# Optimization experiments

Hardware: AMD Instinct MI355X
Metric: run time of the kernel (lower is better)

Reference implementation:

```python
import jax, jax.numpy as jnp
import numpy as np

N_IN, M_MID = 512, 256
B, H, W = 16, 64, 64

def setup_inputs() -> dict:
    key = jax.random.key(0)
    ks = jax.random.split(key, 7)
    s = 0.05
    return {
        "x": jax.random.normal(ks[0], (B, N_IN, H, W), dtype=jnp.float32),
        "W_state": jax.random.normal(ks[1], (M_MID, N_IN), dtype=jnp.float32) * s,
        "b_state": jax.random.normal(ks[2], (M_MID,), dtype=jnp.float32) * s,
        "W_proj": jax.random.normal(ks[3], (M_MID, N_IN), dtype=jnp.float32) * s,
        "b_proj": jax.random.normal(ks[4], (M_MID,), dtype=jnp.float32) * s,
        "W_extend": jax.random.normal(ks[5], (N_IN, M_MID), dtype=jnp.float32) * s,
        "b_extend": jax.random.normal(ks[6], (N_IN,), dtype=jnp.float32) * s,
    }

def reference(x, W_state, b_state, W_proj, b_proj, W_extend, b_extend):
    n, c, h, w = x.shape
    hw = h * w
    xf = x.reshape(n, c, hw)                                   # [n, C, HW]
    # 1x1 convs are channel GEMMs over flattened spatial dim
    x_state = jnp.einsum('mc,nch->nmh', W_state, xf) + b_state[None, :, None]   # [n, M, HW]
    x_proj = jnp.einsum('mc,nch->nmh', W_proj, xf) + b_proj[None, :, None]      # [n, M, HW]
    # bmm -> scale -> softmax -> bmm (graph reasoning over M x M)
    scores = jnp.einsum('nmh,nkh->nmk', x_state, x_proj) / jnp.sqrt(jnp.float32(hw))
    attn = jax.nn.softmax(scores, axis=2)                      # [n, M, M]
    x_rstate = jnp.einsum('nmk,nkh->nmh', attn, x_proj)        # [n, M, HW]
    # extend back to C channels + residual
    ext = jnp.einsum('cm,nmh->nch', W_extend, x_rstate) + b_extend[None, :, None]
    return x + ext.reshape(n, c, h, w)
```

## Files before the change

kernel.cpp:

```cpp
#include <hip/hip_runtime.h>
#include <hip/hip_bf16.h>
#include <stdint.h>

typedef __bf16 bf16x8_t __attribute__((ext_vector_type(8)));
typedef float  f32x4_t  __attribute__((ext_vector_type(4)));
typedef short  short8_t __attribute__((ext_vector_type(8)));

__device__ __forceinline__ unsigned short f2b(float f) {
    union { float f; unsigned u; } v; v.f = f;
    unsigned u = v.u;
    return (unsigned short)((u + 0x7FFFu + ((u >> 16) & 1u)) >> 16);
}
__device__ __forceinline__ float b2f(unsigned short b) {
    union { unsigned u; float f; } v; v.u = ((unsigned)b) << 16; return v.f;
}

#define AS3(p) ((__attribute__((address_space(3))) void*)(p))
#define AS1(p) ((const __attribute__((address_space(1))) void*)(p))
#define FENCE() asm volatile("" ::: "memory")

#define NB   16
#define CIN  512
#define MMID 256
#define HW   4096
#define KSPLIT 4
#define ASZ  (128 * 64)
#define ASZA3 (256 * 64)
#define ASZB3 (64 * 64)

__device__ __forceinline__ void swz3(int gx, int gy, int& bx, int& by, int& bz) {
    const int nwg = gridDim.x, ord = blockIdx.x, q = nwg >> 3;
    const int s = (ord & 7) * q + (ord >> 3);
    by = s % gy;
    const int rem = s / gy;
    bx = rem % gx;
    bz = rem / gx;
}

__global__ __launch_bounds__(256) void prep_weights(
    const float* __restrict__ Ws, const float* __restrict__ Wp,
    const float* __restrict__ Wef, const float* __restrict__ bs,
    const float* __restrict__ bp,
    unsigned short* __restrict__ Wsp, unsigned short* __restrict__ Wex,
    unsigned short* __restrict__ WpT, float* __restrict__ bsp)
{
    int i = blockIdx.x * 256 + threadIdx.x;
    if (i < MMID * CIN) {
        Wsp[i]              = f2b(Ws[i]);
        Wsp[MMID * CIN + i] = f2b(Wp[i]);
        Wex[i]              = f2b(Wef[i]);
        const int c = i >> 8, k = i & (MMID - 1);
        WpT[i] = f2b(Wp[(size_t)k * CIN + c]);
    }
    if (i < MMID) { bsp[i] = bs[i]; bsp[MMID + i] = bp[i]; }
}

__global__ __launch_bounds__(256) void transpose_convert_x(
    const float* __restrict__ x, unsigned short* __restrict__ xT)
{
    __shared__ unsigned short tile[64][66];
    const int n = blockIdx.z, c0 = blockIdx.y * 64, h0 = blockIdx.x * 64;
    const float* s = x + ((size_t)n * CIN + c0) * HW + h0;
    unsigned short* d = xT + ((size_t)n * HW + h0) * CIN + c0;
    const int t = threadIdx.x;
    {
        const int rr = t >> 4, cc = (t & 15) * 4;
        #pragma unroll
        for (int p = 0; p < 4; ++p) {
            int r = p * 16 + rr;
            float4 v = *(const float4*)(s + (size_t)r * HW + cc);
            tile[r][cc + 0] = f2b(v.x); tile[r][cc + 1] = f2b(v.y);
            tile[r][cc + 2] = f2b(v.z); tile[r][cc + 3] = f2b(v.w);
        }
    }
    __syncthreads();
    {
        const int wr = t >> 3, wc = (t & 7) * 8;
        #pragma unroll
        for (int p = 0; p < 2; ++p) {
            int h = p * 32 + wr;
            unsigned short tmp[8];
            #pragma unroll
            for (int j = 0; j < 8; ++j) tmp[j] = tile[wc + j][h];
            *(short8_t*)(d + (size_t)h * CIN + wc) = *(const short8_t*)tmp;
        }
    }
}

__global__ __launch_bounds__(256) void transpose_bf16_64(
    const unsigned short* __restrict__ src, unsigned short* __restrict__ dst,
    int srs, int drs, long long sbs, long long dbs)
{
    __shared__ unsigned short tile[64][66];
    const int n = blockIdx.z, r0 = blockIdx.y * 64, c0 = blockIdx.x * 64;
    const unsigned short* s = src + (size_t)n * sbs + (size_t)r0 * srs + c0;
    unsigned short* d = dst + (size_t)n * dbs + (size_t)c0 * drs + r0;
    const int t = threadIdx.x;
    const int rr = t >> 3, cc = (t & 7) * 8;
    #pragma unroll
    for (int p = 0; p < 2; ++p) {
        int r = p * 32 + rr;
        short8_t v = *(const short8_t*)(s + (size_t)r * srs + cc);
        #pragma unroll
        for (int j = 0; j < 8; ++j) tile[r][cc + j] = ((const unsigned short*)&v)[j];
    }
    __syncthreads();
    #pragma unroll
    for (int p = 0; p < 2; ++p) {
        int c = p * 32 + rr;
        unsigned short tmp[8];
        #pragma unroll
        for (int j = 0; j < 8; ++j) tmp[j] = tile[cc + j][c];
        *(short8_t*)(d + (size_t)c * drs + cc) = *(const short8_t*)tmp;
    }
}

template <int EPI>
__device__ __forceinline__ void epilogue_repack(
    f32x4_t (&acc)[4][4], unsigned short* smem,
    int m0, int n0, int wave, int lane,
    void* __restrict__ Cout, int ldc, size_t cbase)
{
    float* fbuf = (float*)smem;
    const int t   = wave * 64 + lane;
    const int l15 = lane & 15, l16 = lane >> 4;
    const int wr2 = wave >> 1;
    const int wc  = (wave & 1) * 64;

    #pragma unroll
    for (int p = 0; p < 4; ++p) {
        __syncthreads();
        if (wr2 == (p >> 1)) {
            const int ihalf = p & 1;
            #pragma unroll
            for (int i2 = 0; i2 < 2; ++i2) {
                const int i = ihalf * 2 + i2;
                #pragma unroll
                for (int r = 0; r < 4; ++r) {
                    const int lrow = i2 * 16 + l16 * 4 + r;
                    #pragma unroll
                    for (int j = 0; j < 4; ++j)
                        fbuf[lrow * 132 + wc + j * 16 + l15] = acc[i][j][r];
                }
            }
        }
        __syncthreads();
        #pragma unroll
        for (int it = 0; it < 2; ++it) {
            const int lrow = it * 16 + (t >> 4);
            const int col  = (t & 15) * 8;
            const int row  = m0 + p * 32 + lrow;
            float v[8];
            *(float4*)&v[0] = *(const float4*)&fbuf[lrow * 132 + col];
            *(float4*)&v[4] = *(const float4*)&fbuf[lrow * 132 + col + 4];
            const size_t idx = cbase + (size_t)row * ldc + n0 + col;
            if constexpr (EPI == 1) {
                float* op = (float*)Cout + idx;
                *(float4*)op = *(const float4*)&v[0];
                *(float4*)(op + 4) = *(const float4*)&v[4];
            } else if constexpr (EPI == 4) {
                unsigned short o[8];
                #pragma unroll
                for (int k = 0; k < 8; ++k)
                    o[k] = f2b(v[k] + ((row == n0 + col + k) ? 1.0f : 0.0f));
                *(short8_t*)((unsigned short*)Cout + idx) = *(const short8_t*)o;
            } else {
                unsigned short o[8];
                #pragma unroll
                for (int k = 0; k < 8; ++k) o[k] = f2b(v[k]);
                *(short8_t*)((unsigned short*)Cout + idx) = *(const short8_t*)o;
            }
        }
    }
}

#define GEMM_KLOOP(Ab, Bb, lda, ldb, KBEG, NT)                                          \
    auto stage = [&](int k0, int b) {                                                   \
        unsigned short* Asb = smem + b * 2 * ASZ;                                       \
        unsigned short* Bsb = Asb + ASZ;                                                \
        _Pragma("unroll")                                                               \
        for (int c = 0; c < 4; ++c) {                                                   \
            const int o   = (c * 256 + t) * 16;                                         \
            const int row = o >> 7;                                                     \
            const int ce  = ((o & 127) ^ ((row & 7) << 4)) >> 1;                        \
            __builtin_amdgcn_global_load_lds(                                           \
                AS1(Ab + (size_t)row * lda + k0 + ce), AS3((char*)Asb + o), 16, 0, 0);  \
            __builtin_amdgcn_global_load_lds(                                           \
                AS1(Bb + (size_t)row * ldb + k0 + ce), AS3((char*)Bsb + o), 16, 0, 0);  \
        }                                                                               \
    };                                                                                  \
    stage(KBEG, 0);                                                                     \
    for (int itk = 0; itk < (NT); ++itk) {                                              \
        const int cur = itk & 1;                                                        \
        if (itk + 1 < (NT)) {                                                           \
            stage(KBEG + (itk + 1) * 64, cur ^ 1);                                      \
            asm volatile("s_waitcnt vmcnt(8)" ::: "memory");                            \
        } else {                                                                        \
            asm volatile("s_waitcnt vmcnt(0)" ::: "memory");                            \
        }                                                                               \
        __builtin_amdgcn_s_barrier();                                                   \
        FENCE();                                                                        \
        const char* Asb = (const char*)(smem + cur * 2 * ASZ);                          \
        const char* Bsb = Asb + 2 * ASZ;                                                \
        const int swz = (l15 & 7) << 4;                                                 \
        _Pragma("unroll")                                                               \
        for (int ks = 0; ks < 2; ++ks) {                                                \
            bf16x8_t af[4], bfr[4];                                                     \
            const int cb = (ks * 64 + l16 * 16) ^ swz;                                  \
            _Pragma("unroll")                                                           \
            for (int i = 0; i < 4; ++i) {                                               \
                af[i]  = *(const bf16x8_t*)(Asb + (wr + i * 16 + l15) * 128 + cb);      \
                bfr[i] = *(const bf16x8_t*)(Bsb + (wc + i * 16 + l15) * 128 + cb);      \
            }                                                                           \
            _Pragma("unroll")                                                           \
            for (int i = 0; i < 4; ++i)                                                 \
                _Pragma("unroll")                                                       \
                for (int j = 0; j < 4; ++j)                                             \
                    acc[i][j] = __builtin_amdgcn_mfma_f32_16x16x32_bf16(                \
                        af[i], bfr[j], acc[i][j], 0, 0, 0);                             \
        }                                                                               \
        FENCE();                                                                        \
        __builtin_amdgcn_s_barrier();                                                   \
        FENCE();                                                                        \
    }

template <int EPI>
__global__ __launch_bounds__(256, 2) void gemm_occ2(
    const unsigned short* __restrict__ A, const unsigned short* __restrict__ B,
    long long strideA, long long strideB,
    const float* __restrict__ bias, int bias_bstride,
    void* __restrict__ Cout, int ldc, long long strideC,
    int gx, int gy)
{
    __shared__ unsigned short smem[2 * (ASZA3 + ASZB3)];

    int bx, by, n;  swz3(gx, gy, bx, by, n);
    const int m0 = by * 256;
    const int n0 = bx * 64;

    const unsigned short* Ab = A + (size_t)n * strideA + (size_t)m0 * CIN;
    const unsigned short* Bb = B + (size_t)n * strideB + (size_t)n0 * CIN;

    const int t    = threadIdx.x;
    const int lane = t & 63;
    const int wave = t >> 6;
    const int wr   = wave * 64;
    const int l15  = lane & 15;
    const int l16  = lane >> 4;

    f32x4_t acc[4][4] = {};

    auto stage = [&](int k0, int b) {
        unsigned short* Asb = smem + b * (ASZA3 + ASZB3);
        unsigned short* Bsb = Asb + ASZA3;
        #pragma unroll
        for (int c = 0; c < 8; ++c) {
            const int o   = (c * 256 + t) * 16;
            const int row = o >> 7;
            const int ce  = ((o & 127) ^ ((row & 7) << 4)) >> 1;
            __builtin_amdgcn_global_load_lds(
                AS1(Ab + (size_t)row * CIN + k0 + ce), AS3((char*)Asb + o), 16, 0, 0);
        }
        #pragma unroll
        for (int c = 0; c < 2; ++c) {
            const int o   = (c * 256 + t) * 16;
            const int row = o >> 7;
            const int ce  = ((o & 127) ^ ((row & 7) << 4)) >> 1;
            __builtin_amdgcn_global_load_lds(
                AS1(Bb + (size_t)row * CIN + k0 + ce), AS3((char*)Bsb + o), 16, 0, 0);
        }
    };

    const int NT = CIN / 64;
    stage(0, 0);
    for (int itk = 0; itk < NT; ++itk) {
        const int cur = itk & 1;
        if (itk + 1 < NT) {
            stage((itk + 1) * 64, cur ^ 1);
            asm volatile("s_waitcnt vmcnt(10)" ::: "memory");
        } else {
            asm volatile("s_waitcnt vmcnt(0)" ::: "memory");
        }
        __builtin_amdgcn_s_barrier();
        FENCE();
        const char* Asb = (const char*)(smem + cur * (ASZA3 + ASZB3));
        const char* Bsb = Asb + 2 * ASZA3;
        const int swz = (l15 & 7) << 4;
        #pragma unroll
        for (int ks = 0; ks < 2; ++ks) {
            const int cb = (ks * 64 + l16 * 16) ^ swz;
            bf16x8_t af[4], bfr[4];
            #pragma unroll
            for (int i = 0; i < 4; ++i)
                af[i] = *(const bf16x8_t*)(Asb + (wr + i * 16 + l15) * 128 + cb);
            #pragma unroll
            for (int j = 0; j < 4; ++j)
                bfr[j] = *(const bf16x8_t*)(Bsb + (j * 16 + l15) * 128 + cb);
            #pragma unroll
            for (int i = 0; i < 4; ++i)
                #pragma unroll
                for (int j = 0; j < 4; ++j)
                    acc[i][j] = __builtin_amdgcn_mfma_f32_16x16x32_bf16(
                        af[i], bfr[j], acc[i][j], 0, 0, 0);
        }
        FENCE();
        __builtin_amdgcn_s_barrier();
        FENCE();
    }

    float* fbuf = (float*)smem;
    const size_t cbase = (size_t)n * strideC;
    const float* beff = bias + (size_t)n * bias_bstride;
    #pragma unroll
    for (int p = 0; p < 8; ++p) {
        __syncthreads();
        if (wave == (p >> 1)) {
            #pragma unroll
            for (int i2 = 0; i2 < 2; ++i2) {
                const int i = (p & 1) * 2 + i2;
                #pragma unroll
                for (int r = 0; r < 4; ++r) {
                    const int lrow = i2 * 16 + l16 * 4 + r;
                    #pragma unroll
                    for (int j = 0; j < 4; ++j)
                        fbuf[lrow * 68 + j * 16 + l15] = acc[i][j][r];
                }
            }
        }
        __syncthreads();
        const int lrow = t >> 3;
        const int col  = (t & 7) * 8;
        const int row  = m0 + p * 32 + lrow;
        float v[8];
        *(float4*)&v[0] = *(const float4*)&fbuf[lrow * 68 + col];
        *(float4*)&v[4] = *(const float4*)&fbuf[lrow * 68 + col + 4];
        const float badd = beff[row];
        const size_t idx = cbase + (size_t)row * ldc + n0 + col;
        if constexpr (EPI == 1) {
            float o[8];
            #pragma unroll
            for (int k = 0; k < 8; ++k) o[k] = v[k] + badd;
            float* op = (float*)Cout + idx;
            *(float4*)op = *(const float4*)&o[0];
            *(float4*)(op + 4) = *(const float4*)&o[4];
        } else {
            unsigned short o[8];
            #pragma unroll
            for (int k = 0; k < 8; ++k) o[k] = f2b(v[k] + badd);
            *(short8_t*)((unsigned short*)Cout + idx) = *(const short8_t*)o;
        }
    }
}

__global__ __launch_bounds__(256) void gemm_scores(
    const unsigned short* __restrict__ Ysp, float* __restrict__ scoresP)
{
    __shared__ unsigned short smem[4 * ASZ];

    int bx, by, z;  swz3(MMID / 128, MMID / 128, bx, by, z);
    const int n  = z >> 2;
    const int kc = z & 3;
    const int m0 = by * 128;
    const int n0 = bx * 128;

    const unsigned short* Ab = Ysp + (size_t)n * CIN * HW + (size_t)m0 * HW;
    const unsigned short* Bb = Ysp + (size_t)n * CIN * HW + (size_t)(MMID + n0) * HW;

    const int t    = threadIdx.x;
    const int lane = t & 63;
    const int wave = t >> 6;
    const int wr   = (wave >> 1) * 64;
    const int wc   = (wave & 1) * 64;
    const int l15  = lane & 15;
    const int l16  = lane >> 4;

    f32x4_t acc[4][4] = {};
    const int kbeg = kc * (HW / KSPLIT);
    GEMM_KLOOP(Ab, Bb, HW, HW, kbeg, (HW / KSPLIT) / 64)

    float* outp = scoresP + (size_t)(kc * NB + n) * MMID * MMID;
    epilogue_repack<1>(acc, smem, m0, n0, wave, lane, outp, MMID, 0);
}

__global__ __launch_bounds__(256) void softmax_rows(
    const float* __restrict__ scoresP, unsigned short* __restrict__ attn)
{
    const int wave = threadIdx.x >> 6;
    const int l    = threadIdx.x & 63;
    const size_t row = (size_t)blockIdx.x * 4 + wave;
    const size_t pstride = (size_t)NB * MMID * MMID;
    float4 v = {0.f, 0.f, 0.f, 0.f};
    #pragma unroll
    for (int p = 0; p < KSPLIT; ++p) {
        float4 u = *(const float4*)(scoresP + p * pstride + row * MMID + l * 4);
        v.x += u.x; v.y += u.y; v.z += u.z; v.w += u.w;
    }
    float mx = fmaxf(fmaxf(v.x, v.y), fmaxf(v.z, v.w));
    #pragma unroll
    for (int off = 32; off; off >>= 1) mx = fmaxf(mx, __shfl_xor(mx, off));
    const float sc = 0.015625f;
    float e0 = __expf((v.x - mx) * sc), e1 = __expf((v.y - mx) * sc);
    float e2 = __expf((v.z - mx) * sc), e3 = __expf((v.w - mx) * sc);
    float sum = e0 + e1 + e2 + e3;
    #pragma unroll
    for (int off = 32; off; off >>= 1) sum += __shfl_xor(sum, off);
    const float inv = 1.0f / sum;
    unsigned short o[4] = { f2b(e0 * inv), f2b(e1 * inv), f2b(e2 * inv), f2b(e3 * inv) };
    *(uint64_t*)(attn + row * MMID + l * 4) = *(const uint64_t*)o;
}

__global__ __launch_bounds__(256) void compute_vec(
    const unsigned short* __restrict__ G, const float* __restrict__ bsp,
    const float* __restrict__ be, float* __restrict__ vec)
{
    const int n = blockIdx.x >> 1;
    const int c = ((blockIdx.x & 1) << 8) + threadIdx.x;
    const unsigned short* g = G + ((size_t)n * CIN + c) * MMID;
    float s = 0.f;
    for (int k = 0; k < MMID; k += 8) {
        short8_t v = *(const short8_t*)(g + k);
        #pragma unroll
        for (int j = 0; j < 8; ++j)
            s += b2f((unsigned short)v[j]) * bsp[MMID + k + j];
    }
    vec[n * CIN + c] = be[c] + s;
}

template <int EPI>
__global__ __launch_bounds__(256) void gemm_nt(
    const unsigned short* __restrict__ A, const unsigned short* __restrict__ B,
    int lda, int ldb, int K,
    long long strideA, long long strideB,
    void* __restrict__ Cout, int ldc, long long strideC,
    int gx, int gy)
{
    __shared__ unsigned short smem[4 * ASZ];

    int bx, by, n;  swz3(gx, gy, bx, by, n);
    const int m0 = by * 128;
    const int n0 = bx * 128;

    const unsigned short* Ab = A + (size_t)n * strideA + (size_t)m0 * lda;
    const unsigned short* Bb = B + (size_t)n * strideB + (size_t)n0 * ldb;

    const int t    = threadIdx.x;
    const int lane = t & 63;
    const int wave = t >> 6;
    const int wr   = (wave >> 1) * 64;
    const int wc   = (wave & 1) * 64;
    const int l15  = lane & 15;
    const int l16  = lane >> 4;

    f32x4_t acc[4][4] = {};
    GEMM_KLOOP(Ab, Bb, lda, ldb, 0, K / 64)

    epilogue_repack<EPI>(acc, smem, m0, n0, wave, lane,
                         Cout, ldc, (size_t)n * strideC);
}

extern "C" void kernel_launch(void* const* d_in, const int* in_sizes, int n_in,
                              void* d_out, int out_size, void* d_ws, size_t ws_size,
                              hipStream_t stream)
{
    const float* x   = (const float*)d_in[0];
    const float* Ws  = (const float*)d_in[1];
    const float* bs  = (const float*)d_in[2];
    const float* Wp  = (const float*)d_in[3];
    const float* bp  = (const float*)d_in[4];
    const float* Wef = (const float*)d_in[5];
    const float* be  = (const float*)d_in[6];
    float* out = (float*)d_out;

    unsigned short* xT   = (unsigned short*)d_ws;
    unsigned short* Ysp  = xT   + (size_t)NB * HW * CIN;
    unsigned short* Wsp  = Ysp  + (size_t)NB * CIN * HW;
    unsigned short* Wex  = Wsp  + (size_t)CIN * CIN;
    unsigned short* WpT  = Wex  + (size_t)CIN * MMID;
    unsigned short* attn = WpT  + (size_t)CIN * MMID;
    unsigned short* attnT= attn + (size_t)NB * MMID * MMID;
    unsigned short* G    = attnT+ (size_t)NB * MMID * MMID;
    unsigned short* Meff = G    + (size_t)NB * CIN * MMID;
    float* scoresP = (float*)(Meff + (size_t)NB * CIN * CIN);
    float* bsp = scoresP + (size_t)KSPLIT * NB * MMID * MMID;
    float* vec = bsp + CIN;

    prep_weights<<<512, 256, 0, stream>>>(Ws, Wp, Wef, bs, bp, Wsp, Wex, WpT, bsp);

    transpose_convert_x<<<dim3(HW / 64, CIN / 64, NB), 256, 0, stream>>>(x, xT);

    gemm_occ2<0><<<(CIN / 256) * (HW / 64) * NB, 256, 0, stream>>>(
        Wsp, xT, 0LL, (long long)HW * CIN,
        bsp, 0, Ysp, HW, (long long)CIN * HW,
        HW / 64, CIN / 256);

    gemm_scores<<<(MMID / 128) * (MMID / 128) * NB * KSPLIT, 256, 0, stream>>>(
        Ysp, scoresP);

    softmax_rows<<<NB * MMID / 4, 256, 0, stream>>>(scoresP, attn);

    transpose_bf16_64<<<dim3(MMID / 64, MMID / 64, NB), 256, 0, stream>>>(
        attn, attnT, MMID, MMID, (long long)MMID * MMID, (long long)MMID * MMID);

    gemm_nt<2><<<(MMID / 128) * (CIN / 128) * NB, 256, 0, stream>>>(
        Wex, attnT, MMID, MMID, MMID,
        0LL, (long long)MMID * MMID,
        G, MMID, (long long)CIN * MMID,
        MMID / 128, CIN / 128);

    compute_vec<<<NB * 2, 256, 0, stream>>>(G, bsp, be, vec);

    gemm_nt<4><<<(CIN / 128) * (CIN / 128) * NB, 256, 0, stream>>>(
        G, WpT, MMID, MMID, MMID,
        (long long)CIN * MMID, 0LL,
        Meff, CIN, (long long)CIN * CIN,
        CIN / 128, CIN / 128);

    gemm_occ2<1><<<(CIN / 256) * (HW / 64) * NB, 256, 0, stream>>>(
        Meff, xT, (long long)CIN * CIN, (long long)HW * CIN,
        vec, CIN, out, HW, (long long)CIN * HW,
        HW / 64, CIN / 256);
}
```

Measured before the change: 197.4 us.

## Keep B tile stationary in LDS and stream A from global per wave

The two big channel GEMMs are replaced by a kernel that loads the whole 64-column x 512-K slice of B into LDS once and covers all 512 output rows per block with 8 waves. Each wave streams its A fragments directly from global memory (L2-resident weights) instead of staging them through double-buffered LDS. This removes the per-k-step barriers and redundant B reloads across row tiles and halves the grid. The cost is 64KB of LDS per block and uncoalesced direct global A loads with no prefetching, and __launch_bounds__(512,4) may put pressure on registers.

Result: slower. 260.7 us (+32.1%).

```diff
diff --git a/kernel.cpp b/kernel.cpp
--- a/kernel.cpp
+++ b/kernel.cpp
@@ -25,8 +25,6 @@
 #define HW   4096
 #define KSPLIT 4
 #define ASZ  (128 * 64)
-#define ASZA3 (256 * 64)
-#define ASZB3 (64 * 64)
 
 __device__ __forceinline__ void swz3(int gx, int gy, int& bx, int& by, int& bz) {
     const int nwg = gridDim.x, ord = blockIdx.x, q = nwg >> 3;
@@ -225,129 +223,97 @@
     }
 
 template <int EPI>
-__global__ __launch_bounds__(256, 2) void gemm_occ2(
+__global__ __launch_bounds__(512, 4) void gemm_bstat(
     const unsigned short* __restrict__ A, const unsigned short* __restrict__ B,
     long long strideA, long long strideB,
     const float* __restrict__ bias, int bias_bstride,
-    void* __restrict__ Cout, int ldc, long long strideC,
-    int gx, int gy)
-{
-    __shared__ unsigned short smem[2 * (ASZA3 + ASZB3)];
-
-    int bx, by, n;  swz3(gx, gy, bx, by, n);
-    const int m0 = by * 256;
+    void* __restrict__ Cout, int ldc, long long strideC, int gx)
+{
+    __shared__ unsigned short smem[64 * 512];
+
+    int bx, by, n;  swz3(gx, 1, bx, by, n);
     const int n0 = bx * 64;
 
-    const unsigned short* Ab = A + (size_t)n * strideA + (size_t)m0 * CIN;
     const unsigned short* Bb = B + (size_t)n * strideB + (size_t)n0 * CIN;
 
     const int t    = threadIdx.x;
     const int lane = t & 63;
     const int wave = t >> 6;
-    const int wr   = wave * 64;
     const int l15  = lane & 15;
     const int l16  = lane >> 4;
 
+    #pragma unroll
+    for (int c = 0; c < 8; ++c) {
+        const int o   = (c * 512 + t) * 16;
+        const int row = o >> 10;
+        const int ce  = ((o & 1023) ^ ((row & 7) << 4)) >> 1;
+        __builtin_amdgcn_global_load_lds(
+            AS1(Bb + (size_t)row * CIN + ce), AS3((char*)smem + o), 16, 0, 0);
+    }
+    asm volatile("s_waitcnt vmcnt(0)" ::: "memory");
+    __syncthreads();
+    FENCE();
+
+    const unsigned short* Aw = A + (size_t)n * strideA
+                               + (size_t)(wave * 64 + l15) * CIN + l16 * 8;
+    const char* Bs = (const char*)smem;
+    const int swz = (l15 & 7) << 4;
+
     f32x4_t acc[4][4] = {};
-
-    auto stage = [&](int k0, int b) {
-        unsigned short* Asb = smem + b * (ASZA3 + ASZB3);
-        unsigned short* Bsb = Asb + ASZA3;
-        #pragma unroll
-        for (int c = 0; c < 8; ++c) {
-            const int o   = (c * 256 + t) * 16;
-            const int row = o >> 7;
-            const int ce  = ((o & 127) ^ ((row & 7) << 4)) >> 1;
-            __builtin_amdgcn_global_load_lds(
-                AS1(Ab + (size_t)row * CIN + k0 + ce), AS3((char*)Asb + o), 16, 0, 0);
-        }
-        #pragma unroll
-        for (int c = 0; c < 2; ++c) {
-            const int o   = (c * 256 + t) * 16;
-            const int row = o >> 7;
-            const int ce  = ((o & 127) ^ ((row & 7) << 4)) >> 1;
-            __builtin_amdgcn_global_load_lds(
-                AS1(Bb + (size_t)row * CIN + k0 + ce), AS3((char*)Bsb + o), 16, 0, 0);
-        }
-    };
-
-    const int NT = CIN / 64;
-    stage(0, 0);
-    for (int itk = 0; itk < NT; ++itk) {
-        const int cur = itk & 1;
-        if (itk + 1 < NT) {
-            stage((itk + 1) * 64, cur ^ 1);
-            asm volatile("s_waitcnt vmcnt(10)" ::: "memory");
-        } else {
-            asm volatile("s_waitcnt vmcnt(0)" ::: "memory");
-        }
-        __builtin_amdgcn_s_barrier();
-        FENCE();
-        const char* Asb = (const char*)(smem + cur * (ASZA3 + ASZB3));
-        const char* Bsb = Asb + 2 * ASZA3;
-        const int swz = (l15 & 7) << 4;
-        #pragma unroll
-        for (int ks = 0; ks < 2; ++ks) {
-            const int cb = (ks * 64 + l16 * 16) ^ swz;
-            bf16x8_t af[4], bfr[4];
-            #pragma unroll
-            for (int i = 0; i < 4; ++i)
-                af[i] = *(const bf16x8_t*)(Asb + (wr + i * 16 + l15) * 128 + cb);
+    #pragma unroll 2
+    for (int kt = 0; kt < 16; ++kt) {
+        bf16x8_t af[4], bfr[4];
+        #pragma unroll
+        for (int i = 0; i < 4; ++i)
+            af[i] = *(const bf16x8_t*)(Aw + (size_t)i * 16 * CIN + kt * 32);
+        #pragma unroll
+        for (int j = 0; j < 4; ++j)
+            bfr[j] = *(const bf16x8_t*)(Bs + (j * 16 + l15) * 1024
+                                          + ((kt * 64 + l16 * 16) ^ swz));
+        #pragma unroll
+        for (int i = 0; i < 4; ++i)
             #pragma unroll
             for (int j = 0; j < 4; ++j)
-                bfr[j] = *(const bf16x8_t*)(Bsb + (j * 16 + l15) * 128 + cb);
+                acc[i][j] = __builtin_amdgcn_mfma_f32_16x16x32_bf16(
+                    af[i], bfr[j], acc[i][j], 0, 0, 0);
+    }
+
+    float* fbuf = (float*)smem;
+    const size_t cbase = (size_t)n * strideC;
+    const float* beff = bias + (size_t)n * bias_bstride;
+    #pragma unroll
+    for (int p = 0; p < 4; ++p) {
+        __syncthreads();
+        if ((wave >> 1) == p) {
+            const int wsub = wave & 1;
             #pragma unroll
             for (int i = 0; i < 4; ++i)
                 #pragma unroll
-                for (int j = 0; j < 4; ++j)
-                    acc[i][j] = __builtin_amdgcn_mfma_f32_16x16x32_bf16(
-                        af[i], bfr[j], acc[i][j], 0, 0, 0);
-        }
-        FENCE();
-        __builtin_amdgcn_s_barrier();
-        FENCE();
-    }
-
-    float* fbuf = (float*)smem;
-    const size_t cbase = (size_t)n * strideC;
-    const float* beff = bias + (size_t)n * bias_bstride;
-    #pragma unroll
-    for (int p = 0; p < 8; ++p) {
-        __syncthreads();
-        if (wave == (p >> 1)) {
-            #pragma unroll
-            for (int i2 = 0; i2 < 2; ++i2) {
-                const int i = (p & 1) * 2 + i2;
-                #pragma unroll
                 for (int r = 0; r < 4; ++r) {
-                    const int lrow = i2 * 16 + l16 * 4 + r;
+                    const int lrow = wsub * 64 + i * 16 + l16 * 4 + r;
                     #pragma unroll
                     for (int j = 0; j < 4; ++j)
                         fbuf[lrow * 68 + j * 16 + l15] = acc[i][j][r];
                 }
+        }
+        __syncthreads();
+        #pragma unroll
+        for (int q = 0; q < 4; ++q) {
+            const int lrow = q * 32 + (t >> 4);
+            const int col  = (t & 15) * 4;
+            const int row  = p * 128 + lrow;
+            float4 v = *(const float4*)&fbuf[lrow * 68 + col];
+            const float badd = beff[row];
+            const size_t idx = cbase + (size_t)row * ldc + n0 + col;
+            if constexpr (EPI == 1) {
+                float4 o; o.x = v.x + badd; o.y = v.y + badd;
+                o.z = v.z + badd; o.w = v.w + badd;
+                *(float4*)((float*)Cout + idx) = o;
+            } else {
+                unsigned short o[4] = { f2b(v.x + badd), f2b(v.y + badd),
+                                        f2b(v.z + badd), f2b(v.w + badd) };
+                *(uint64_t*)((unsigned short*)Cout + idx) = *(const uint64_t*)o;
             }
-        }
-        __syncthreads();
-        const int lrow = t >> 3;
-        const int col  = (t & 7) * 8;
-        const int row  = m0 + p * 32 + lrow;
-        float v[8];
-        *(float4*)&v[0] = *(const float4*)&fbuf[lrow * 68 + col];
-        *(float4*)&v[4] = *(const float4*)&fbuf[lrow * 68 + col + 4];
-        const float badd = beff[row];
-        const size_t idx = cbase + (size_t)row * ldc + n0 + col;
-        if constexpr (EPI == 1) {
-            float o[8];
-            #pragma unroll
-            for (int k = 0; k < 8; ++k) o[k] = v[k] + badd;
-            float* op = (float*)Cout + idx;
-            *(float4*)op = *(const float4*)&o[0];
-            *(float4*)(op + 4) = *(const float4*)&o[4];
-        } else {
-            unsigned short o[8];
-            #pragma unroll
-            for (int k = 0; k < 8; ++k) o[k] = f2b(v[k] + badd);
-            *(short8_t*)((unsigned short*)Cout + idx) = *(const short8_t*)o;
         }
     }
 }
@@ -488,10 +454,9 @@
 
     transpose_convert_x<<<dim3(HW / 64, CIN / 64, NB), 256, 0, stream>>>(x, xT);
 
-    gemm_occ2<0><<<(CIN / 256) * (HW / 64) * NB, 256, 0, stream>>>(
+    gemm_bstat<0><<<(HW / 64) * NB, 512, 0, stream>>>(
         Wsp, xT, 0LL, (long long)HW * CIN,
-        bsp, 0, Ysp, HW, (long long)CIN * HW,
-        HW / 64, CIN / 256);
+        bsp, 0, Ysp, HW, (long long)CIN * HW, HW / 64);
 
     gemm_scores<<<(MMID / 128) * (MMID / 128) * NB * KSPLIT, 256, 0, stream>>>(
         Ysp, scoresP);
@@ -515,8 +480,7 @@
         Meff, CIN, (long long)CIN * CIN,
         CIN / 128, CIN / 128);
 
-    gemm_occ2<1><<<(CIN / 256) * (HW / 64) * NB, 256, 0, stream>>>(
+    gemm_bstat<1><<<(HW / 64) * NB, 512, 0, stream>>>(
         Meff, xT, (long long)CIN * CIN, (long long)HW * CIN,
-        vec, CIN, out, HW, (long long)CIN * HW,
-        HW / 64, CIN / 256);
-}
+        vec, CIN, out, HW, (long long)CIN * HW, HW / 64);
+}
```

## Replace two-wave-occupancy GEMM with 8-wave 256x128 tile and triple-buffered pipeline

Applied to the files above, without the earlier changes.

The two large channel GEMMs (state/proj projection and the final extend GEMM) now run in a 512-thread, 8-wave kernel with a 256x128 output tile instead of 256x64. A three-slot LDS ring is used, with the next-next k-tile's global-to-LDS loads split into two parts and issued between the fragment reads and the MFMA phases. s_setprio is raised around the MFMA bursts. The aim is more reuse per loaded A tile and better hiding of load latency. In exchange the kernel drops to one block per CU with 144KB of LDS, and the epilogue is reorganized into two larger passes.

Measured after the change: 223.1 us. +13.0%, slower.

```diff
diff --git a/kernel.cpp b/kernel.cpp
--- a/kernel.cpp
+++ b/kernel.cpp
@@ -25,8 +25,7 @@
 #define HW   4096
 #define KSPLIT 4
 #define ASZ  (128 * 64)
-#define ASZA3 (256 * 64)
-#define ASZB3 (64 * 64)
+#define SLOT_E 24576
 
 __device__ __forceinline__ void swz3(int gx, int gy, int& bx, int& by, int& bz) {
     const int nwg = gridDim.x, ord = blockIdx.x, q = nwg >> 3;
@@ -225,18 +224,18 @@
     }
 
 template <int EPI>
-__global__ __launch_bounds__(256, 2) void gemm_occ2(
+__global__ __launch_bounds__(512, 1) void gemm8p(
     const unsigned short* __restrict__ A, const unsigned short* __restrict__ B,
     long long strideA, long long strideB,
     const float* __restrict__ bias, int bias_bstride,
     void* __restrict__ Cout, int ldc, long long strideC,
     int gx, int gy)
 {
-    __shared__ unsigned short smem[2 * (ASZA3 + ASZB3)];
+    __shared__ unsigned short smem[3 * SLOT_E];
 
     int bx, by, n;  swz3(gx, gy, bx, by, n);
     const int m0 = by * 256;
-    const int n0 = bx * 64;
+    const int n0 = bx * 128;
 
     const unsigned short* Ab = A + (size_t)n * strideA + (size_t)m0 * CIN;
     const unsigned short* Bb = B + (size_t)n * strideB + (size_t)n0 * CIN;
@@ -244,111 +243,134 @@
     const int t    = threadIdx.x;
     const int lane = t & 63;
     const int wave = t >> 6;
-    const int wr   = wave * 64;
+    const int wr   = (wave >> 1) * 64;
+    const int wc   = (wave & 1) * 64;
     const int l15  = lane & 15;
     const int l16  = lane >> 4;
+    const int swz  = (l15 & 7) << 4;
+
+    auto stage_part = [&](int ktile, int slot, int part) {
+        unsigned short* Asb = smem + slot * SLOT_E;
+        unsigned short* Bsb = Asb + 16384;
+        if (part == 0) {
+            #pragma unroll
+            for (int c = 0; c < 3; ++c) {
+                const int o   = (c * 512 + t) * 16;
+                const int row = o >> 7;
+                const int ce  = ((o & 127) ^ ((row & 7) << 4)) >> 1;
+                __builtin_amdgcn_global_load_lds(
+                    AS1(Ab + (size_t)row * CIN + ktile * 64 + ce),
+                    AS3((char*)Asb + o), 16, 0, 0);
+            }
+        } else {
+            {
+                const int o   = (3 * 512 + t) * 16;
+                const int row = o >> 7;
+                const int ce  = ((o & 127) ^ ((row & 7) << 4)) >> 1;
+                __builtin_amdgcn_global_load_lds(
+                    AS1(Ab + (size_t)row * CIN + ktile * 64 + ce),
+                    AS3((char*)Asb + o), 16, 0, 0);
+            }
+            #pragma unroll
+            for (int c = 0; c < 2; ++c) {
+                const int o   = (c * 512 + t) * 16;
+                const int row = o >> 7;
+                const int ce  = ((o & 127) ^ ((row & 7) << 4)) >> 1;
+                __builtin_amdgcn_global_load_lds(
+                    AS1(Bb + (size_t)row * CIN + ktile * 64 + ce),
+                    AS3((char*)Bsb + o), 16, 0, 0);
+            }
+        }
+    };
 
     f32x4_t acc[4][4] = {};
 
-    auto stage = [&](int k0, int b) {
-        unsigned short* Asb = smem + b * (ASZA3 + ASZB3);
-        unsigned short* Bsb = Asb + ASZA3;
-        #pragma unroll
-        for (int c = 0; c < 8; ++c) {
-            const int o   = (c * 256 + t) * 16;
-            const int row = o >> 7;
-            const int ce  = ((o & 127) ^ ((row & 7) << 4)) >> 1;
-            __builtin_amdgcn_global_load_lds(
-                AS1(Ab + (size_t)row * CIN + k0 + ce), AS3((char*)Asb + o), 16, 0, 0);
-        }
-        #pragma unroll
-        for (int c = 0; c < 2; ++c) {
-            const int o   = (c * 256 + t) * 16;
-            const int row = o >> 7;
-            const int ce  = ((o & 127) ^ ((row & 7) << 4)) >> 1;
-            __builtin_amdgcn_global_load_lds(
-                AS1(Bb + (size_t)row * CIN + k0 + ce), AS3((char*)Bsb + o), 16, 0, 0);
-        }
-    };
-
-    const int NT = CIN / 64;
-    stage(0, 0);
-    for (int itk = 0; itk < NT; ++itk) {
-        const int cur = itk & 1;
-        if (itk + 1 < NT) {
-            stage((itk + 1) * 64, cur ^ 1);
-            asm volatile("s_waitcnt vmcnt(10)" ::: "memory");
-        } else {
-            asm volatile("s_waitcnt vmcnt(0)" ::: "memory");
-        }
-        __builtin_amdgcn_s_barrier();
-        FENCE();
-        const char* Asb = (const char*)(smem + cur * (ASZA3 + ASZB3));
-        const char* Bsb = Asb + 2 * ASZA3;
-        const int swz = (l15 & 7) << 4;
-        #pragma unroll
-        for (int ks = 0; ks < 2; ++ks) {
-            const int cb = (ks * 64 + l16 * 16) ^ swz;
+    stage_part(0, 0, 0); stage_part(0, 0, 1);
+    stage_part(1, 1, 0); stage_part(1, 1, 1);
+    asm volatile("s_waitcnt vmcnt(6)" ::: "memory");
+    __builtin_amdgcn_s_barrier();
+    FENCE();
+
+    for (int kt = 0; kt < 8; ++kt) {
+        const int slot  = kt % 3;
+        const int nslot = (kt + 2) % 3;
+        const char* Asb = (const char*)(smem + slot * SLOT_E);
+        const char* Bsb = Asb + 32768;
+        #pragma unroll
+        for (int ph = 0; ph < 2; ++ph) {
+            const int cb = (ph * 64 + l16 * 16) ^ swz;
             bf16x8_t af[4], bfr[4];
             #pragma unroll
             for (int i = 0; i < 4; ++i)
                 af[i] = *(const bf16x8_t*)(Asb + (wr + i * 16 + l15) * 128 + cb);
             #pragma unroll
             for (int j = 0; j < 4; ++j)
-                bfr[j] = *(const bf16x8_t*)(Bsb + (j * 16 + l15) * 128 + cb);
+                bfr[j] = *(const bf16x8_t*)(Bsb + (wc + j * 16 + l15) * 128 + cb);
+            if (kt < 6) stage_part(kt + 2, nslot, ph);
+            __builtin_amdgcn_s_setprio(1);
             #pragma unroll
             for (int i = 0; i < 4; ++i)
                 #pragma unroll
                 for (int j = 0; j < 4; ++j)
                     acc[i][j] = __builtin_amdgcn_mfma_f32_16x16x32_bf16(
                         af[i], bfr[j], acc[i][j], 0, 0, 0);
-        }
-        FENCE();
-        __builtin_amdgcn_s_barrier();
-        FENCE();
+            __builtin_amdgcn_s_setprio(0);
+            if (ph == 1) {
+                if (kt < 6) { asm volatile("s_waitcnt vmcnt(6)" ::: "memory"); }
+                else        { asm volatile("s_waitcnt vmcnt(0)" ::: "memory"); }
+            }
+            FENCE();
+            __builtin_amdgcn_s_barrier();
+            FENCE();
+        }
     }
 
     float* fbuf = (float*)smem;
     const size_t cbase = (size_t)n * strideC;
     const float* beff = bias + (size_t)n * bias_bstride;
     #pragma unroll
-    for (int p = 0; p < 8; ++p) {
-        __syncthreads();
-        if (wave == (p >> 1)) {
-            #pragma unroll
-            for (int i2 = 0; i2 < 2; ++i2) {
-                const int i = (p & 1) * 2 + i2;
+    for (int p = 0; p < 2; ++p) {
+        if ((wave >> 2) == p) {
+            const int lr0 = ((wave >> 1) & 1) * 64;
+            #pragma unroll
+            for (int i = 0; i < 4; ++i)
                 #pragma unroll
                 for (int r = 0; r < 4; ++r) {
-                    const int lrow = i2 * 16 + l16 * 4 + r;
+                    const int lrow = lr0 + i * 16 + l16 * 4 + r;
                     #pragma unroll
                     for (int j = 0; j < 4; ++j)
-                        fbuf[lrow * 68 + j * 16 + l15] = acc[i][j][r];
+                        fbuf[lrow * 132 + wc + j * 16 + l15] = acc[i][j][r];
                 }
-            }
         }
         __syncthreads();
-        const int lrow = t >> 3;
-        const int col  = (t & 7) * 8;
-        const int row  = m0 + p * 32 + lrow;
-        float v[8];
-        *(float4*)&v[0] = *(const float4*)&fbuf[lrow * 68 + col];
-        *(float4*)&v[4] = *(const float4*)&fbuf[lrow * 68 + col + 4];
-        const float badd = beff[row];
-        const size_t idx = cbase + (size_t)row * ldc + n0 + col;
-        if constexpr (EPI == 1) {
-            float o[8];
-            #pragma unroll
-            for (int k = 0; k < 8; ++k) o[k] = v[k] + badd;
-            float* op = (float*)Cout + idx;
-            *(float4*)op = *(const float4*)&o[0];
-            *(float4*)(op + 4) = *(const float4*)&o[4];
-        } else {
-            unsigned short o[8];
-            #pragma unroll
-            for (int k = 0; k < 8; ++k) o[k] = f2b(v[k] + badd);
-            *(short8_t*)((unsigned short*)Cout + idx) = *(const short8_t*)o;
-        }
+        #pragma unroll
+        for (int it = 0; it < 2; ++it) {
+            const int lrow = it * 64 + (t >> 3);
+            const int col  = (t & 7) * 16;
+            const int row  = m0 + p * 128 + lrow;
+            const float badd = beff[row];
+            float v[16];
+            #pragma unroll
+            for (int q = 0; q < 4; ++q)
+                *(float4*)&v[q * 4] = *(const float4*)&fbuf[lrow * 132 + col + q * 4];
+            const size_t idx = cbase + (size_t)row * ldc + n0 + col;
+            if constexpr (EPI == 1) {
+                #pragma unroll
+                for (int q = 0; q < 4; ++q) {
+                    float4 o;
+                    o.x = v[q*4+0] + badd; o.y = v[q*4+1] + badd;
+                    o.z = v[q*4+2] + badd; o.w = v[q*4+3] + badd;
+                    *(float4*)((float*)Cout + idx + q * 4) = o;
+                }
+            } else {
+                unsigned short o[16];
+                #pragma unroll
+                for (int k = 0; k < 16; ++k) o[k] = f2b(v[k] + badd);
+                *(short8_t*)((unsigned short*)Cout + idx)     = *(const short8_t*)&o[0];
+                *(short8_t*)((unsigned short*)Cout + idx + 8) = *(const short8_t*)&o[8];
+            }
+        }
+        __syncthreads();
     }
 }
 
@@ -488,10 +510,10 @@
 
     transpose_convert_x<<<dim3(HW / 64, CIN / 64, NB), 256, 0, stream>>>(x, xT);
 
-    gemm_occ2<0><<<(CIN / 256) * (HW / 64) * NB, 256, 0, stream>>>(
+    gemm8p<0><<<(HW / 128) * (CIN / 256) * NB, 512, 0, stream>>>(
         Wsp, xT, 0LL, (long long)HW * CIN,
         bsp, 0, Ysp, HW, (long long)CIN * HW,
-        HW / 64, CIN / 256);
+        HW / 128, CIN / 256);
 
     gemm_scores<<<(MMID / 128) * (MMID / 128) * NB * KSPLIT, 256, 0, stream>>>(
         Ysp, scoresP);
@@ -515,8 +537,8 @@
         Meff, CIN, (long long)CIN * CIN,
         CIN / 128, CIN / 128);
 
-    gemm_occ2<1><<<(CIN / 256) * (HW / 64) * NB, 256, 0, stream>>>(
+    gemm8p<1><<<(HW / 128) * (CIN / 256) * NB, 512, 0, stream>>>(
         Meff, xT, (long long)CIN * CIN, (long long)HW * CIN,
         vec, CIN, out, HW, (long long)CIN * HW,
-        HW / 64, CIN / 256);
-}
+        HW / 128, CIN / 256);
+}
```

## Halve GEMM K-tile for 4-block occupancy and fuse attn transpose into softmax

Applied to the files above, without the earlier changes.

The main 256x64 GEMM kernel now uses a 32-wide K tile, which halves LDS per block, and requests 4 blocks per CU instead of 2. It uses a 4-row XOR swizzle and raises wave priority around the MFMA block. Each tile now gets half as much MFMA work per barrier, so sync overhead per FLOP goes up while occupancy and latency hiding improve. Separately, softmax writes the transposed attention directly with strided 2-byte scattered stores, which removes the extra transpose kernel launch.

Result: slower. 212.1 us (+7.4%).

```diff
diff --git a/kernel.cpp b/kernel.cpp
--- a/kernel.cpp
+++ b/kernel.cpp
@@ -25,8 +25,8 @@
 #define HW   4096
 #define KSPLIT 4
 #define ASZ  (128 * 64)
-#define ASZA3 (256 * 64)
-#define ASZB3 (64 * 64)
+#define A3E  (256 * 32)
+#define B3E  (64 * 32)
 
 __device__ __forceinline__ void swz3(int gx, int gy, int& bx, int& by, int& bz) {
     const int nwg = gridDim.x, ord = blockIdx.x, q = nwg >> 3;
@@ -84,34 +84,6 @@
             for (int j = 0; j < 8; ++j) tmp[j] = tile[wc + j][h];
             *(short8_t*)(d + (size_t)h * CIN + wc) = *(const short8_t*)tmp;
         }
-    }
-}
-
-__global__ __launch_bounds__(256) void transpose_bf16_64(
-    const unsigned short* __restrict__ src, unsigned short* __restrict__ dst,
-    int srs, int drs, long long sbs, long long dbs)
-{
-    __shared__ unsigned short tile[64][66];
-    const int n = blockIdx.z, r0 = blockIdx.y * 64, c0 = blockIdx.x * 64;
-    const unsigned short* s = src + (size_t)n * sbs + (size_t)r0 * srs + c0;
-    unsigned short* d = dst + (size_t)n * dbs + (size_t)c0 * drs + r0;
-    const int t = threadIdx.x;
-    const int rr = t >> 3, cc = (t & 7) * 8;
-    #pragma unroll
-    for (int p = 0; p < 2; ++p) {
-        int r = p * 32 + rr;
-        short8_t v = *(const short8_t*)(s + (size_t)r * srs + cc);
-        #pragma unroll
-        for (int j = 0; j < 8; ++j) tile[r][cc + j] = ((const unsigned short*)&v)[j];
-    }
-    __syncthreads();
-    #pragma unroll
-    for (int p = 0; p < 2; ++p) {
-        int c = p * 32 + rr;
-        unsigned short tmp[8];
-        #pragma unroll
-        for (int j = 0; j < 8; ++j) tmp[j] = tile[cc + j][c];
-        *(short8_t*)(d + (size_t)c * drs + cc) = *(const short8_t*)tmp;
     }
 }
 
@@ -225,14 +197,14 @@
     }
 
 template <int EPI>
-__global__ __launch_bounds__(256, 2) void gemm_occ2(
+__global__ __launch_bounds__(256, 4) void gemm_occ4(
     const unsigned short* __restrict__ A, const unsigned short* __restrict__ B,
     long long strideA, long long strideB,
     const float* __restrict__ bias, int bias_bstride,
     void* __restrict__ Cout, int ldc, long long strideC,
     int gx, int gy)
 {
-    __shared__ unsigned short smem[2 * (ASZA3 + ASZB3)];
+    __shared__ unsigned short smem[2 * (A3E + B3E)];
 
     int bx, by, n;  swz3(gx, gy, bx, by, n);
     const int m0 = by * 256;
@@ -251,58 +223,58 @@
     f32x4_t acc[4][4] = {};
 
     auto stage = [&](int k0, int b) {
-        unsigned short* Asb = smem + b * (ASZA3 + ASZB3);
-        unsigned short* Bsb = Asb + ASZA3;
-        #pragma unroll
-        for (int c = 0; c < 8; ++c) {
+        unsigned short* Asb = smem + b * (A3E + B3E);
+        unsigned short* Bsb = Asb + A3E;
+        #pragma unroll
+        for (int c = 0; c < 4; ++c) {
             const int o   = (c * 256 + t) * 16;
-            const int row = o >> 7;
-            const int ce  = ((o & 127) ^ ((row & 7) << 4)) >> 1;
+            const int row = o >> 6;
+            const int ce  = ((o & 63) ^ ((row & 3) << 4)) >> 1;
             __builtin_amdgcn_global_load_lds(
                 AS1(Ab + (size_t)row * CIN + k0 + ce), AS3((char*)Asb + o), 16, 0, 0);
         }
-        #pragma unroll
-        for (int c = 0; c < 2; ++c) {
-            const int o   = (c * 256 + t) * 16;
-            const int row = o >> 7;
-            const int ce  = ((o & 127) ^ ((row & 7) << 4)) >> 1;
+        {
+            const int o   = t * 16;
+            const int row = o >> 6;
+            const int ce  = ((o & 63) ^ ((row & 3) << 4)) >> 1;
             __builtin_amdgcn_global_load_lds(
                 AS1(Bb + (size_t)row * CIN + k0 + ce), AS3((char*)Bsb + o), 16, 0, 0);
         }
     };
 
-    const int NT = CIN / 64;
+    const int NT = CIN / 32;
     stage(0, 0);
     for (int itk = 0; itk < NT; ++itk) {
         const int cur = itk & 1;
         if (itk + 1 < NT) {
-            stage((itk + 1) * 64, cur ^ 1);
-            asm volatile("s_waitcnt vmcnt(10)" ::: "memory");
+            stage((itk + 1) * 32, cur ^ 1);
+            asm volatile("s_waitcnt vmcnt(5)" ::: "memory");
         } else {
             asm volatile("s_waitcnt vmcnt(0)" ::: "memory");
         }
         __builtin_amdgcn_s_barrier();
         FENCE();
-        const char* Asb = (const char*)(smem + cur * (ASZA3 + ASZB3));
-        const char* Bsb = Asb + 2 * ASZA3;
-        const int swz = (l15 & 7) << 4;
-        #pragma unroll
-        for (int ks = 0; ks < 2; ++ks) {
-            const int cb = (ks * 64 + l16 * 16) ^ swz;
-            bf16x8_t af[4], bfr[4];
-            #pragma unroll
-            for (int i = 0; i < 4; ++i)
-                af[i] = *(const bf16x8_t*)(Asb + (wr + i * 16 + l15) * 128 + cb);
+        const char* Asb = (const char*)(smem + cur * (A3E + B3E));
+        const char* Bsb = Asb + 2 * A3E;
+        bf16x8_t af[4], bfr[4];
+        #pragma unroll
+        for (int i = 0; i < 4; ++i) {
+            const int row = wr + i * 16 + l15;
+            af[i] = *(const bf16x8_t*)(Asb + row * 64 + ((l16 * 16) ^ ((row & 3) << 4)));
+        }
+        #pragma unroll
+        for (int j = 0; j < 4; ++j) {
+            const int row = j * 16 + l15;
+            bfr[j] = *(const bf16x8_t*)(Bsb + row * 64 + ((l16 * 16) ^ ((row & 3) << 4)));
+        }
+        __builtin_amdgcn_s_setprio(1);
+        #pragma unroll
+        for (int i = 0; i < 4; ++i)
             #pragma unroll
             for (int j = 0; j < 4; ++j)
-                bfr[j] = *(const bf16x8_t*)(Bsb + (j * 16 + l15) * 128 + cb);
-            #pragma unroll
-            for (int i = 0; i < 4; ++i)
-                #pragma unroll
-                for (int j = 0; j < 4; ++j)
-                    acc[i][j] = __builtin_amdgcn_mfma_f32_16x16x32_bf16(
-                        af[i], bfr[j], acc[i][j], 0, 0, 0);
-        }
+                acc[i][j] = __builtin_amdgcn_mfma_f32_16x16x32_bf16(
+                    af[i], bfr[j], acc[i][j], 0, 0, 0);
+        __builtin_amdgcn_s_setprio(0);
         FENCE();
         __builtin_amdgcn_s_barrier();
         FENCE();
@@ -383,11 +355,14 @@
 }
 
 __global__ __launch_bounds__(256) void softmax_rows(
-    const float* __restrict__ scoresP, unsigned short* __restrict__ attn)
+    const float* __restrict__ scoresP, unsigned short* __restrict__ attn,
+    unsigned short* __restrict__ attnT)
 {
     const int wave = threadIdx.x >> 6;
     const int l    = threadIdx.x & 63;
     const size_t row = (size_t)blockIdx.x * 4 + wave;
+    const int nb = (int)(row >> 8);
+    const int m  = (int)(row & 255);
     const size_t pstride = (size_t)NB * MMID * MMID;
     float4 v = {0.f, 0.f, 0.f, 0.f};
     #pragma unroll
@@ -407,6 +382,9 @@
     const float inv = 1.0f / sum;
     unsigned short o[4] = { f2b(e0 * inv), f2b(e1 * inv), f2b(e2 * inv), f2b(e3 * inv) };
     *(uint64_t*)(attn + row * MMID + l * 4) = *(const uint64_t*)o;
+    unsigned short* aT = attnT + (size_t)nb * MMID * MMID + m;
+    #pragma unroll
+    for (int j = 0; j < 4; ++j) aT[(size_t)(l * 4 + j) * MMID] = o[j];
 }
 
 __global__ __launch_bounds__(256) void compute_vec(
@@ -488,7 +466,7 @@
 
     transpose_convert_x<<<dim3(HW / 64, CIN / 64, NB), 256, 0, stream>>>(x, xT);
 
-    gemm_occ2<0><<<(CIN / 256) * (HW / 64) * NB, 256, 0, stream>>>(
+    gemm_occ4<0><<<(CIN / 256) * (HW / 64) * NB, 256, 0, stream>>>(
         Wsp, xT, 0LL, (long long)HW * CIN,
         bsp, 0, Ysp, HW, (long long)CIN * HW,
         HW / 64, CIN / 256);
@@ -496,10 +474,7 @@
     gemm_scores<<<(MMID / 128) * (MMID / 128) * NB * KSPLIT, 256, 0, stream>>>(
         Ysp, scoresP);
 
-    softmax_rows<<<NB * MMID / 4, 256, 0, stream>>>(scoresP, attn);
-
-    transpose_bf16_64<<<dim3(MMID / 64, MMID / 64, NB), 256, 0, stream>>>(
-        attn, attnT, MMID, MMID, (long long)MMID * MMID, (long long)MMID * MMID);
+    softmax_rows<<<NB * MMID / 4, 256, 0, stream>>>(scoresP, attn, attnT);
 
     gemm_nt<2><<<(MMID / 128) * (CIN / 128) * NB, 256, 0, stream>>>(
         Wex, attnT, MMID, MMID, MMID,
@@ -515,7 +490,7 @@
         Meff, CIN, (long long)CIN * CIN,
         CIN / 128, CIN / 128);
 
-    gemm_occ2<1><<<(CIN / 256) * (HW / 64) * NB, 256, 0, stream>>>(
+    gemm_occ4<1><<<(CIN / 256) * (HW / 64) * NB, 256, 0, stream>>>(
         Meff, xT, (long long)CIN * CIN, (long long)HW * CIN,
         vec, CIN, out, HW, (long long)CIN * HW,
         HW / 64, CIN / 256);
```
